# Kernel tuning notes

Measured on AMD Instinct MI355X. Metric: run time of the kernel, lower is better.

Reference implementation:

```python
import jax, jax.numpy as jnp
import numpy as np

T, H_IN = 2048, 84
HID = 256
NA = 18


def _conv(x, w, b, stride):
    # x: [N,C,H,W], w: [O,I,kh,kw]
    y = jax.lax.conv_general_dilated(
        x, w, window_strides=(stride, stride), padding='VALID',
        dimension_numbers=('NCHW', 'OIHW', 'NCHW'))
    return jax.nn.relu(y + b[None, :, None, None])


def setup_inputs() -> dict:
    key = jax.random.key(0)
    ks = jax.random.split(key, 17)
    p = lambda k, shape, s=0.05: (jax.random.normal(k, shape, jnp.float32) * s)
    return {
        'input_frames': jax.random.uniform(ks[0], (T, 1, H_IN, H_IN), jnp.float32),
        'conv1_w': p(ks[1], (32, 1, 8, 8)),   'conv1_b': p(ks[2], (32,)),
        'conv2_w': p(ks[3], (64, 32, 4, 4)),  'conv2_b': p(ks[4], (64,)),
        'conv3_w': p(ks[5], (256, 64, 3, 3)), 'conv3_b': p(ks[6], (256,)),
        'attn_w1': p(ks[7], (HID, HID)),      'attn_b1': p(ks[8], (HID,)),
        'attn_w2': p(ks[9], (HID, HID)),      'attn_b2': p(ks[10], (HID,)),
        'lstm_w_ih': p(ks[11], (4 * HID, HID)), 'lstm_w_hh': p(ks[12], (4 * HID, HID)),
        'lstm_b_ih': p(ks[13], (4 * HID,)),     'lstm_b_hh': p(ks[14], (4 * HID,)),
        'q_w': p(ks[15], (NA, HID)),          'q_b': p(ks[16], (NA,)),
    }


def reference(input_frames, conv1_w, conv1_b, conv2_w, conv2_b, conv3_w, conv3_b,
              attn_w1, attn_b1, attn_w2, attn_b2,
              lstm_w_ih, lstm_w_hh, lstm_b_ih, lstm_b_hh, q_w, q_b):
    # CNN over all frames at once (loop in torch was over frames; math identical)
    x = _conv(input_frames, conv1_w, conv1_b, 4)   # [T,32,20,20]
    x = _conv(x, conv2_w, conv2_b, 2)              # [T,64,9,9]
    fm = _conv(x, conv3_w, conv3_b, 1)             # [T,256,7,7]
    t, c, hh, ww = fm.shape
    # build_vector: vectors[i, ch] = fm[ch, y, x], i = y*W + x
    vecs = fm.reshape(t, c, hh * ww).transpose(0, 2, 1)  # [T,49,256]

    def step(carry, v):
        h, cc = carry  # [256], [256]
        # additive attention; softmax over the 256 feature dim per spatial vector
        s = jnp.tanh(v @ attn_w1.T + attn_b1 + h)              # [49,256]
        w = jax.nn.softmax(s @ attn_w2.T + attn_b2, axis=-1)   # [49,256]
        ctx = jnp.sum(w * v, axis=0)                           # [256]
        # single-layer LSTM cell, torch gate order i,f,g,o
        gates = ctx @ lstm_w_ih.T + lstm_b_ih + h @ lstm_w_hh.T + lstm_b_hh
        i, f, g, o = jnp.split(gates, 4)
        c_new = jax.nn.sigmoid(f) * cc + jax.nn.sigmoid(i) * jnp.tanh(g)
        h_new = jax.nn.sigmoid(o) * jnp.tanh(c_new)
        return (h_new, c_new), None

    h0 = jnp.zeros((HID,), fm.dtype)
    (h_T, _), _ = jax.lax.scan(step, (h0, h0), vecs)
    q = h_T @ q_w.T + q_b          # [18]
    return q[None, :]              # [1, nr_actions], matches torch output
```

## Files before the change

### kernel.cpp

```cpp
#include <hip/hip_runtime.h>
#include <hip/hip_bf16.h>
#include <math.h>


#define T_FRAMES 2048
#define NI 49
#define HID 256
#define NA 18
#define NWG 8

typedef __bf16 v8bf __attribute__((ext_vector_type(8)));
typedef float v4f __attribute__((ext_vector_type(4)));

static constexpr size_t OFF_FM1   = 0;
static constexpr size_t OFF_FM2   = 104857600;
static constexpr size_t OFF_VECS  = 147324928;
static constexpr size_t OFF_W2B   = 250085376;
static constexpr size_t OFF_WIHB  = OFF_W2B  + 131072;
static constexpr size_t OFF_WHHB  = OFF_WIHB + 524288;
static constexpr size_t OFF_W1T   = OFF_WHHB + 524288;
static constexpr size_t OFF_HBUF  = OFF_FM2;
static constexpr size_t OFF_CPUB  = OFF_FM2 + 2048;

__global__ void prep_weights(const float* __restrict__ w2, const float* __restrict__ wih,
                             const float* __restrict__ whh, const float* __restrict__ w1,
                             __bf16* w2b, __bf16* wihb, __bf16* whhb, float* w1t) {
  int idx = blockIdx.x * 256 + threadIdx.x;
  int stride = gridDim.x * 256;
  for (int i = idx; i < 65536; i += stride) w2b[i] = (__bf16)w2[i];
  for (int i = idx; i < 262144; i += stride) wihb[i] = (__bf16)wih[i];
  for (int i = idx; i < 262144; i += stride) whhb[i] = (__bf16)whh[i];
  for (int i = idx; i < 65536; i += stride) {
    int r = i >> 8, c = i & 255;
    w1t[c * 256 + r] = w1[i];
  }
}

__global__ void conv1_k(const float* __restrict__ x, const float* __restrict__ w,
                        const float* __restrict__ b, float* __restrict__ y) {
  int idx = blockIdx.x * 256 + threadIdx.x;
  if (idx >= T_FRAMES * 32 * 20 * 20) return;
  int xx = idx % 20, yy = (idx / 20) % 20, o = (idx / 400) % 32, t = idx / 12800;
  const float* xp = x + t * 7056 + yy * 4 * 84 + xx * 4;
  const float* wp = w + o * 64;
  float acc = b[o];
  #pragma unroll
  for (int ky = 0; ky < 8; ky++)
    #pragma unroll
    for (int kx = 0; kx < 8; kx++)
      acc += xp[ky * 84 + kx] * wp[ky * 8 + kx];
  y[idx] = fmaxf(acc, 0.f);
}

__global__ __launch_bounds__(256) void conv2_k(const float* __restrict__ fm1, const float* __restrict__ w,
                                               const float* __restrict__ b, float* __restrict__ fm2) {
  __shared__ float xs[32 * 400];
  int t = blockIdx.x, tid = threadIdx.x;
  for (int i = tid; i < 12800; i += 256) xs[i] = fm1[t * 12800 + i];
  __syncthreads();
  int o = tid >> 2, q = tid & 3;
  int p0 = q * 21, p1 = (p0 + 21 < 81) ? p0 + 21 : 81;
  int ob[21];
  #pragma unroll
  for (int i2 = 0; i2 < 21; i2++) {
    int p = p0 + i2; if (p > 80) p = 80;
    int yy = p / 9, xx2 = p - yy * 9;
    ob[i2] = yy * 40 + xx2 * 2;
  }
  float acc[21];
  #pragma unroll
  for (int i2 = 0; i2 < 21; i2++) acc[i2] = 0.f;
  for (int c = 0; c < 32; c++) {
    int cbase = c * 400;
    for (int ky = 0; ky < 4; ky++)
      for (int kx = 0; kx < 4; kx++) {
        float wgt = w[((o * 32 + c) * 4 + ky) * 4 + kx];
        int kyo = ky * 20 + kx;
        #pragma unroll
        for (int i2 = 0; i2 < 21; i2++)
          acc[i2] += wgt * xs[cbase + ob[i2] + kyo];
      }
  }
  float bo = b[o];
  #pragma unroll
  for (int i2 = 0; i2 < 21; i2++) {
    int p = p0 + i2;
    if (p < p1) fm2[t * 5184 + o * 81 + p] = fmaxf(acc[i2] + bo, 0.f);
  }
}

__global__ __launch_bounds__(256) void conv3_k(const float* __restrict__ fm2, const float* __restrict__ w,
                                               const float* __restrict__ b, float* __restrict__ vecs) {
  __shared__ float xs[64 * 81];
  __shared__ float ws4[256][37];
  int t = blockIdx.x, tid = threadIdx.x;
  for (int i = tid; i < 64 * 81; i += 256) xs[i] = fm2[t * 5184 + i];
  float acc[49];
  #pragma unroll
  for (int i = 0; i < 49; i++) acc[i] = 0.f;
  for (int c0 = 0; c0 < 64; c0 += 4) {
    __syncthreads();
    for (int i = tid; i < 256 * 36; i += 256) {
      int oo = i / 36, j = i - oo * 36;
      ws4[oo][j] = w[oo * 576 + c0 * 9 + j];
    }
    __syncthreads();
    for (int cc = 0; cc < 4; cc++)
      for (int ky = 0; ky < 3; ky++)
        for (int kx = 0; kx < 3; kx++) {
          float wgt = ws4[tid][cc * 9 + ky * 3 + kx];
          const float* xp = &xs[(c0 + cc) * 81 + ky * 9 + kx];
          #pragma unroll
          for (int yy = 0; yy < 7; yy++)
            #pragma unroll
            for (int xx = 0; xx < 7; xx++)
              acc[yy * 7 + xx] += wgt * xp[yy * 9 + xx];
        }
  }
  float bo = b[tid];
  for (int i = 0; i < 49; i++)
    vecs[(t * 49 + i) * 256 + tid] = fmaxf(acc[i] + bo, 0.f);
}

__global__ __launch_bounds__(256) void aprep_k(const float* __restrict__ vecs, const float* __restrict__ w1t,
                                               const float* __restrict__ b1, float* __restrict__ A) {
  __shared__ float vs[49][256];
  int t = blockIdx.x, tid = threadIdx.x;
  for (int i = tid; i < 49 * 256; i += 256) vs[i >> 8][i & 255] = vecs[t * 12544 + i];
  __syncthreads();
  float acc[49];
  #pragma unroll
  for (int i = 0; i < 49; i++) acc[i] = 0.f;
  for (int k = 0; k < 256; k++) {
    float wgt = w1t[k * 256 + tid];
    #pragma unroll
    for (int i = 0; i < 49; i++) acc[i] += vs[i][k] * wgt;
  }
  float bb = b1[tid];
  for (int i = 0; i < 49; i++) A[(t * 49 + i) * 256 + tid] = acc[i] + bb;
}

__global__ void init_comm(unsigned long long* hbuf, unsigned long long* cpub) {
  int idx = blockIdx.x * 256 + threadIdx.x;
  if (idx < 256) hbuf[idx] = 0ull;
  if (idx < NWG * 128) cpub[idx] = 0ull;
}

__device__ __forceinline__ float tanh_fast(float x) {
  float e = __expf(2.f * x);
  return 1.f - 2.f * __builtin_amdgcn_rcpf(e + 1.f);
}
__device__ __forceinline__ float sigm_fast(float x) {
  return __builtin_amdgcn_rcpf(1.f + __expf(-x));
}

__global__ __launch_bounds__(256, 1) void scan_k(
    const float* __restrict__ A, const float* __restrict__ vecs,
    const __bf16* __restrict__ w2b, const __bf16* __restrict__ wihb, const __bf16* __restrict__ whhb,
    const float* __restrict__ b2g, const float* __restrict__ bihg, const float* __restrict__ bhhg,
    const float* __restrict__ qw, const float* __restrict__ qb,
    unsigned long long* hbuf, unsigned long long* cpub, float* out) {
  const int w = blockIdx.x;

  __shared__ __bf16 Ss[16][264];
  __shared__ float hs[HID];
  __shared__ __bf16 hbf[HID];
  __shared__ float Wt[8][HID];
  __shared__ float cxp[8][HID];
  __shared__ float b2s[HID];
  __shared__ float gb[4][32];
  __shared__ unsigned cpl[128];

  const int tid = threadIdx.x;
  const int lane = tid & 63;
  const int wv = tid >> 6;
  const int quad = lane >> 4;
  const int l15 = lane & 15;
  const int r0 = 6 * w;
  const int nr = (w < 7) ? 6 : 7;
  const int prow = tid >> 5;
  const int pcol = (tid & 31) * 8;

  for (int i = tid; i < 16 * 264; i += 256) (&Ss[0][0])[i] = (__bf16)0.f;
  for (int i = tid; i < 8 * HID; i += 256) (&cxp[0][0])[i] = 0.f;
  b2s[tid] = b2g[tid];
  hs[tid] = 0.f;
  hbf[tid] = (__bf16)0.f;
  float cbias[4];
  if (tid < 32) {
    #pragma unroll
    for (int g = 0; g < 4; g++) {
      int row = 256 * g + 32 * w + tid;
      cbias[g] = bihg[row] + bhhg[row];
    }
  }
  float creg = 0.f;

  v8bf BW2[4][8];
  #pragma unroll
  for (int ntl = 0; ntl < 4; ntl++) {
    const int row = wv * 64 + ntl * 16 + l15;
    #pragma unroll
    for (int k = 0; k < 8; k++)
      BW2[ntl][k] = *(const v8bf*)(w2b + row * 256 + k * 32 + quad * 8);
  }
  v8bf BIH[2][8], BHH[2][8];
  #pragma unroll
  for (int nt = 0; nt < 2; nt++) {
    const int row = 256 * wv + 32 * w + nt * 16 + l15;
    #pragma unroll
    for (int k = 0; k < 8; k++) {
      BIH[nt][k] = *(const v8bf*)(wihb + row * 256 + k * 32 + quad * 8);
      BHH[nt][k] = *(const v8bf*)(whhb + row * 256 + k * 32 + quad * 8);
    }
  }
  __syncthreads();

  for (int t = 0; t < T_FRAMES; t++) {
    int rr = r0 + prow; if (rr > 48) rr = 48;
    const float* Ap = A + ((long)t * NI + rr) * HID + pcol;
    const float* Vp = vecs + ((long)t * NI + rr) * HID + pcol;
    const float4 a40 = *(const float4*)(Ap);
    const float4 a41 = *(const float4*)(Ap + 4);
    const float4 v40 = *(const float4*)(Vp);
    const float4 v41 = *(const float4*)(Vp + 4);

    if (t > 0) {
      const unsigned tgt = (unsigned)t;
      unsigned long long pk =
          __hip_atomic_load(&hbuf[tid], __ATOMIC_RELAXED, __HIP_MEMORY_SCOPE_AGENT);
      int guard = 0;
      while ((unsigned)(pk >> 32) < tgt && ++guard < 5000000) {
        __builtin_amdgcn_s_sleep(1);
        pk = __hip_atomic_load(&hbuf[tid], __ATOMIC_RELAXED, __HIP_MEMORY_SCOPE_AGENT);
      }
      float hv = __uint_as_float((unsigned)pk);
      hs[tid] = hv;
      hbf[tid] = (__bf16)hv;
      __syncthreads();
    }

    if (prow < nr) {
      const float* hp = &hs[pcol];
      v8bf sv;
      sv[0] = (__bf16)tanh_fast(a40.x + hp[0]);
      sv[1] = (__bf16)tanh_fast(a40.y + hp[1]);
      sv[2] = (__bf16)tanh_fast(a40.z + hp[2]);
      sv[3] = (__bf16)tanh_fast(a40.w + hp[3]);
      sv[4] = (__bf16)tanh_fast(a41.x + hp[4]);
      sv[5] = (__bf16)tanh_fast(a41.y + hp[5]);
      sv[6] = (__bf16)tanh_fast(a41.z + hp[6]);
      sv[7] = (__bf16)tanh_fast(a41.w + hp[7]);
      *(v8bf*)&Ss[prow][pcol] = sv;
    }
    __syncthreads();

    v4f acc[4];
    #pragma unroll
    for (int ntl = 0; ntl < 4; ntl++) acc[ntl] = (v4f){0.f, 0.f, 0.f, 0.f};
    #pragma unroll
    for (int k = 0; k < 8; k++) {
      const v8bf av = *(const v8bf*)&Ss[l15][k * 32 + quad * 8];
      #pragma unroll
      for (int ntl = 0; ntl < 4; ntl++)
        acc[ntl] = __builtin_amdgcn_mfma_f32_16x16x32_bf16(av, BW2[ntl][k], acc[ntl], 0, 0, 0);
    }
    if (quad < 2) {
      #pragma unroll
      for (int ntl = 0; ntl < 4; ntl++) {
        const int col = wv * 64 + ntl * 16 + l15;
        const float bb = b2s[col];
        #pragma unroll
        for (int reg = 0; reg < 4; reg++)
          Wt[quad * 4 + reg][col] = acc[ntl][reg] + bb;
      }
    }
    __syncthreads();

    if (prow < nr) {
      float x[8];
      *(float4*)&x[0] = *(const float4*)&Wt[prow][pcol];
      *(float4*)&x[4] = *(const float4*)&Wt[prow][pcol + 4];
      float m = x[0];
      #pragma unroll
      for (int i = 1; i < 8; i++) m = fmaxf(m, x[i]);
      #pragma unroll
      for (int off = 16; off; off >>= 1) m = fmaxf(m, __shfl_xor(m, off, 64));
      float e[8], sm = 0.f;
      #pragma unroll
      for (int i = 0; i < 8; i++) { e[i] = __expf(x[i] - m); sm += e[i]; }
      #pragma unroll
      for (int off = 16; off; off >>= 1) sm += __shfl_xor(sm, off, 64);
      const float inv = __builtin_amdgcn_rcpf(sm);
      cxp[prow][pcol + 0] = e[0] * inv * v40.x;
      cxp[prow][pcol + 1] = e[1] * inv * v40.y;
      cxp[prow][pcol + 2] = e[2] * inv * v40.z;
      cxp[prow][pcol + 3] = e[3] * inv * v40.w;
      cxp[prow][pcol + 4] = e[4] * inv * v41.x;
      cxp[prow][pcol + 5] = e[5] * inv * v41.y;
      cxp[prow][pcol + 6] = e[6] * inv * v41.z;
      cxp[prow][pcol + 7] = e[7] * inv * v41.w;
    }
    __syncthreads();

    float cp = 0.f;
    #pragma unroll
    for (int r = 0; r < 8; r++) cp += cxp[r][tid];
    float cpo = __shfl_xor(cp, 1, 64);
    if ((tid & 1) == 0) {
      union { __bf16 b; unsigned short s; } lo, hi;
      lo.b = (__bf16)cp; hi.b = (__bf16)cpo;
      unsigned word = ((unsigned)hi.s << 16) | (unsigned)lo.s;
      unsigned long long pk =
          ((unsigned long long)(unsigned)(t + 1) << 32) | (unsigned long long)word;
      __hip_atomic_store(&cpub[w * 128 + (tid >> 1)], pk, __ATOMIC_RELAXED, __HIP_MEMORY_SCOPE_AGENT);
      cpl[tid >> 1] = word;
    }
    __syncthreads();

    v4f gacc[2];
    gacc[0] = (v4f){0.f, 0.f, 0.f, 0.f};
    gacc[1] = (v4f){0.f, 0.f, 0.f, 0.f};
    #pragma unroll
    for (int k = 0; k < 8; k++) {
      v8bf hf;
      #pragma unroll
      for (int z = 0; z < 8; z++) hf[z] = (__bf16)0.f;
      if (l15 == 0) hf = *(const v8bf*)&hbf[k * 32 + quad * 8];
      gacc[0] = __builtin_amdgcn_mfma_f32_16x16x32_bf16(hf, BHH[0][k], gacc[0], 0, 0, 0);
      gacc[1] = __builtin_amdgcn_mfma_f32_16x16x32_bf16(hf, BHH[1][k], gacc[1], 0, 0, 0);
    }

    unsigned long long g[8][4];
    const unsigned ctgt = (unsigned)(t + 1);
    const bool remote = (l15 < NWG) && (l15 != w);
    {
      int guard = 0;
      while (true) {
        bool ok = true;
        if (remote) {
          const unsigned long long* src = cpub + l15 * 128 + quad * 4;
          #pragma unroll
          for (int k = 0; k < 8; k++)
            #pragma unroll
            for (int q2 = 0; q2 < 4; q2++) {
              g[k][q2] = __hip_atomic_load(&src[k * 16 + q2], __ATOMIC_RELAXED, __HIP_MEMORY_SCOPE_AGENT);
              ok &= ((unsigned)(g[k][q2] >> 32) >= ctgt);
            }
        }
        if (__all(ok) || ++guard > 5000000) break;
        __builtin_amdgcn_s_sleep(1);
      }
    }

    #pragma unroll
    for (int k = 0; k < 8; k++) {
      union { unsigned u[4]; v8bf v; } pf;
      if (remote) {
        pf.u[0] = (unsigned)g[k][0]; pf.u[1] = (unsigned)g[k][1];
        pf.u[2] = (unsigned)g[k][2]; pf.u[3] = (unsigned)g[k][3];
      } else if (l15 == w) {
        pf.u[0] = cpl[k * 16 + quad * 4 + 0];
        pf.u[1] = cpl[k * 16 + quad * 4 + 1];
        pf.u[2] = cpl[k * 16 + quad * 4 + 2];
        pf.u[3] = cpl[k * 16 + quad * 4 + 3];
      } else {
        pf.u[0] = pf.u[1] = pf.u[2] = pf.u[3] = 0u;
      }
      gacc[0] = __builtin_amdgcn_mfma_f32_16x16x32_bf16(pf.v, BIH[0][k], gacc[0], 0, 0, 0);
      gacc[1] = __builtin_amdgcn_mfma_f32_16x16x32_bf16(pf.v, BIH[1][k], gacc[1], 0, 0, 0);
    }
    #pragma unroll
    for (int nt = 0; nt < 2; nt++) {
      float tot = gacc[nt][0] + gacc[nt][1] + gacc[nt][2] + gacc[nt][3];
      tot += __shfl_xor(tot, 16, 64);
      tot += __shfl_xor(tot, 32, 64);
      if (lane < 16) gb[wv][nt * 16 + lane] = tot;
    }
    __syncthreads();

    if (tid < 32) {
      float gi = gb[0][tid] + cbias[0];
      float gf = gb[1][tid] + cbias[1];
      float gg = gb[2][tid] + cbias[2];
      float go = gb[3][tid] + cbias[3];
      float si = sigm_fast(gi);
      float sf = sigm_fast(gf);
      float so = sigm_fast(go);
      creg = sf * creg + si * tanh_fast(gg);
      float hn = so * tanh_fast(creg);
      unsigned long long pk = ((unsigned long long)(unsigned)(t + 1) << 32) |
                              (unsigned long long)__float_as_uint(hn);
      __hip_atomic_store(&hbuf[32 * w + tid], pk, __ATOMIC_RELAXED, __HIP_MEMORY_SCOPE_AGENT);
    }
  }

  if (w == 0) {
    const unsigned tgt = (unsigned)T_FRAMES;
    unsigned long long pk =
        __hip_atomic_load(&hbuf[tid], __ATOMIC_RELAXED, __HIP_MEMORY_SCOPE_AGENT);
    int guard = 0;
    while ((unsigned)(pk >> 32) < tgt && ++guard < 5000000) {
      __builtin_amdgcn_s_sleep(1);
      pk = __hip_atomic_load(&hbuf[tid], __ATOMIC_RELAXED, __HIP_MEMORY_SCOPE_AGENT);
    }
    hs[tid] = __uint_as_float((unsigned)pk);
    __syncthreads();
    if (tid < NA) {
      float acc = qb[tid];
      for (int k = 0; k < HID; k++) acc += hs[k] * qw[tid * HID + k];
      out[tid] = acc;
    }
  }
}

extern "C" void kernel_launch(void* const* d_in, const int* in_sizes, int n_in,
                              void* d_out, int out_size, void* d_ws, size_t ws_size,
                              hipStream_t stream) {
  const float* frames = (const float*)d_in[0];
  const float* c1w = (const float*)d_in[1];
  const float* c1b = (const float*)d_in[2];
  const float* c2w = (const float*)d_in[3];
  const float* c2b = (const float*)d_in[4];
  const float* c3w = (const float*)d_in[5];
  const float* c3b = (const float*)d_in[6];
  const float* aw1 = (const float*)d_in[7];
  const float* ab1 = (const float*)d_in[8];
  const float* aw2 = (const float*)d_in[9];
  const float* ab2 = (const float*)d_in[10];
  const float* wih = (const float*)d_in[11];
  const float* whh = (const float*)d_in[12];
  const float* bih = (const float*)d_in[13];
  const float* bhh = (const float*)d_in[14];
  const float* qw  = (const float*)d_in[15];
  const float* qb  = (const float*)d_in[16];

  char* ws = (char*)d_ws;
  float*  fm1   = (float*)(ws + OFF_FM1);
  float*  A     = (float*)(ws + OFF_FM1);
  float*  fm2   = (float*)(ws + OFF_FM2);
  float*  vecs  = (float*)(ws + OFF_VECS);
  __bf16* w2b   = (__bf16*)(ws + OFF_W2B);
  __bf16* wihb  = (__bf16*)(ws + OFF_WIHB);
  __bf16* whhb  = (__bf16*)(ws + OFF_WHHB);
  float*  w1t   = (float*)(ws + OFF_W1T);
  unsigned long long* hbuf = (unsigned long long*)(ws + OFF_HBUF);
  unsigned long long* cpub = (unsigned long long*)(ws + OFF_CPUB);

  prep_weights<<<256, 256, 0, stream>>>(aw2, wih, whh, aw1, w2b, wihb, whhb, w1t);
  conv1_k<<<102400, 256, 0, stream>>>(frames, c1w, c1b, fm1);
  conv2_k<<<T_FRAMES, 256, 0, stream>>>(fm1, c2w, c2b, fm2);
  conv3_k<<<T_FRAMES, 256, 0, stream>>>(fm2, c3w, c3b, vecs);
  aprep_k<<<T_FRAMES, 256, 0, stream>>>(vecs, w1t, ab1, A);
  init_comm<<<4, 256, 0, stream>>>(hbuf, cpub);
  scan_k<<<NWG, 256, 0, stream>>>(A, vecs, w2b, wihb, whhb, ab2, bih, bhh, qw, qb,
                                  hbuf, cpub, (float*)d_out);
}
```

Baseline: 15.29 ms.

## Compute full attention context redundantly per workgroup, dropping cross-workgroup context exchange

Each of the 8 workgroups now computes attention over all 49 spatial rows (four 16-row MFMA tiles) instead of a 6-7 row slice. The per-step exchange of partial context sums through global memory, with its second spin-wait barrier, is removed. Only the hidden-state exchange is left as a cross-workgroup sync per step. The cost is about 8x redundant attention work per workgroup, more global loads per step, and much larger LDS use.

```diff
diff --git a/kernel.cpp b/kernel.cpp
--- a/kernel.cpp
+++ b/kernel.cpp
@@ -19,8 +19,7 @@
 static constexpr size_t OFF_WIHB  = OFF_W2B  + 131072;
 static constexpr size_t OFF_WHHB  = OFF_WIHB + 524288;
 static constexpr size_t OFF_W1T   = OFF_WHHB + 524288;
-static constexpr size_t OFF_HBUF  = OFF_FM2;
-static constexpr size_t OFF_CPUB  = OFF_FM2 + 2048;
+static constexpr size_t OFF_COMM  = OFF_FM2;
 
 __global__ void prep_weights(const float* __restrict__ w2, const float* __restrict__ wih,
                              const float* __restrict__ whh, const float* __restrict__ w1,
@@ -140,10 +139,10 @@
   for (int i = 0; i < 49; i++) A[(t * 49 + i) * 256 + tid] = acc[i] + bb;
 }
 
-__global__ void init_comm(unsigned long long* hbuf, unsigned long long* cpub) {
+__global__ void init_comm(unsigned long long* comm) {
   int idx = blockIdx.x * 256 + threadIdx.x;
-  if (idx < 256) hbuf[idx] = 0ull;
-  if (idx < NWG * 128) cpub[idx] = 0ull;
+  if (idx < 256)
+    __hip_atomic_store(&comm[idx], 0ull, __ATOMIC_RELAXED, __HIP_MEMORY_SCOPE_AGENT);
 }
 
 __device__ __forceinline__ float tanh_fast(float x) {
@@ -159,30 +158,27 @@
     const __bf16* __restrict__ w2b, const __bf16* __restrict__ wihb, const __bf16* __restrict__ whhb,
     const float* __restrict__ b2g, const float* __restrict__ bihg, const float* __restrict__ bhhg,
     const float* __restrict__ qw, const float* __restrict__ qb,
-    unsigned long long* hbuf, unsigned long long* cpub, float* out) {
+    unsigned long long* hbuf, float* out) {
   const int w = blockIdx.x;
 
-  __shared__ __bf16 Ss[16][264];
+  __shared__ __bf16 Ss[64][264];
+  __shared__ float Wt[64][260];
+  __shared__ float cxp[8][HID];
   __shared__ float hs[HID];
   __shared__ __bf16 hbf[HID];
-  __shared__ float Wt[8][HID];
-  __shared__ float cxp[8][HID];
+  __shared__ __bf16 ctxbf[HID];
   __shared__ float b2s[HID];
   __shared__ float gb[4][32];
-  __shared__ unsigned cpl[128];
 
   const int tid = threadIdx.x;
   const int lane = tid & 63;
   const int wv = tid >> 6;
   const int quad = lane >> 4;
   const int l15 = lane & 15;
-  const int r0 = 6 * w;
-  const int nr = (w < 7) ? 6 : 7;
   const int prow = tid >> 5;
   const int pcol = (tid & 31) * 8;
 
-  for (int i = tid; i < 16 * 264; i += 256) (&Ss[0][0])[i] = (__bf16)0.f;
-  for (int i = tid; i < 8 * HID; i += 256) (&cxp[0][0])[i] = 0.f;
+  for (int i = tid; i < 64 * 264; i += 256) (&Ss[0][0])[i] = (__bf16)0.f;
   b2s[tid] = b2g[tid];
   hs[tid] = 0.f;
   hbf[tid] = (__bf16)0.f;
@@ -217,20 +213,26 @@
   __syncthreads();
 
   for (int t = 0; t < T_FRAMES; t++) {
-    int rr = r0 + prow; if (rr > 48) rr = 48;
-    const float* Ap = A + ((long)t * NI + rr) * HID + pcol;
-    const float* Vp = vecs + ((long)t * NI + rr) * HID + pcol;
-    const float4 a40 = *(const float4*)(Ap);
-    const float4 a41 = *(const float4*)(Ap + 4);
-    const float4 v40 = *(const float4*)(Vp);
-    const float4 v41 = *(const float4*)(Vp + 4);
+    const long base = (long)t * NI * HID;
+    float4 aa0[8], aa1[8], vv0[8], vv1[8];
+    #pragma unroll
+    for (int i = 0; i < 8; i++) {
+      int row = prow + 8 * i;
+      int ra = (row < NI) ? row : (NI - 1);
+      const float* Ap = A + base + (long)ra * HID + pcol;
+      const float* Vp = vecs + base + (long)ra * HID + pcol;
+      aa0[i] = *(const float4*)(Ap);
+      aa1[i] = *(const float4*)(Ap + 4);
+      vv0[i] = *(const float4*)(Vp);
+      vv1[i] = *(const float4*)(Vp + 4);
+    }
 
     if (t > 0) {
       const unsigned tgt = (unsigned)t;
       unsigned long long pk =
           __hip_atomic_load(&hbuf[tid], __ATOMIC_RELAXED, __HIP_MEMORY_SCOPE_AGENT);
-      int guard = 0;
-      while ((unsigned)(pk >> 32) < tgt && ++guard < 5000000) {
+      int gd = 0;
+      while ((unsigned)(pk >> 32) != tgt && ++gd < 5000000) {
         __builtin_amdgcn_s_sleep(1);
         pk = __hip_atomic_load(&hbuf[tid], __ATOMIC_RELAXED, __HIP_MEMORY_SCOPE_AGENT);
       }
@@ -240,81 +242,94 @@
       __syncthreads();
     }
 
-    if (prow < nr) {
+    {
       const float* hp = &hs[pcol];
-      v8bf sv;
-      sv[0] = (__bf16)tanh_fast(a40.x + hp[0]);
-      sv[1] = (__bf16)tanh_fast(a40.y + hp[1]);
-      sv[2] = (__bf16)tanh_fast(a40.z + hp[2]);
-      sv[3] = (__bf16)tanh_fast(a40.w + hp[3]);
-      sv[4] = (__bf16)tanh_fast(a41.x + hp[4]);
-      sv[5] = (__bf16)tanh_fast(a41.y + hp[5]);
-      sv[6] = (__bf16)tanh_fast(a41.z + hp[6]);
-      sv[7] = (__bf16)tanh_fast(a41.w + hp[7]);
-      *(v8bf*)&Ss[prow][pcol] = sv;
-    }
-    __syncthreads();
-
-    v4f acc[4];
-    #pragma unroll
-    for (int ntl = 0; ntl < 4; ntl++) acc[ntl] = (v4f){0.f, 0.f, 0.f, 0.f};
-    #pragma unroll
-    for (int k = 0; k < 8; k++) {
-      const v8bf av = *(const v8bf*)&Ss[l15][k * 32 + quad * 8];
-      #pragma unroll
-      for (int ntl = 0; ntl < 4; ntl++)
-        acc[ntl] = __builtin_amdgcn_mfma_f32_16x16x32_bf16(av, BW2[ntl][k], acc[ntl], 0, 0, 0);
-    }
-    if (quad < 2) {
+      float h0 = hp[0], h1 = hp[1], h2 = hp[2], h3 = hp[3];
+      float h4 = hp[4], h5 = hp[5], h6 = hp[6], h7 = hp[7];
+      #pragma unroll
+      for (int i = 0; i < 8; i++) {
+        int row = prow + 8 * i;
+        if (row < NI) {
+          v8bf sv;
+          sv[0] = (__bf16)tanh_fast(aa0[i].x + h0);
+          sv[1] = (__bf16)tanh_fast(aa0[i].y + h1);
+          sv[2] = (__bf16)tanh_fast(aa0[i].z + h2);
+          sv[3] = (__bf16)tanh_fast(aa0[i].w + h3);
+          sv[4] = (__bf16)tanh_fast(aa1[i].x + h4);
+          sv[5] = (__bf16)tanh_fast(aa1[i].y + h5);
+          sv[6] = (__bf16)tanh_fast(aa1[i].z + h6);
+          sv[7] = (__bf16)tanh_fast(aa1[i].w + h7);
+          *(v8bf*)&Ss[row][pcol] = sv;
+        }
+      }
+    }
+    __syncthreads();
+
+    #pragma unroll
+    for (int rt = 0; rt < 4; rt++) {
+      v4f acc[4];
+      #pragma unroll
+      for (int ntl = 0; ntl < 4; ntl++) acc[ntl] = (v4f){0.f, 0.f, 0.f, 0.f};
+      #pragma unroll
+      for (int k = 0; k < 8; k++) {
+        const v8bf av = *(const v8bf*)&Ss[rt * 16 + l15][k * 32 + quad * 8];
+        #pragma unroll
+        for (int ntl = 0; ntl < 4; ntl++)
+          acc[ntl] = __builtin_amdgcn_mfma_f32_16x16x32_bf16(av, BW2[ntl][k], acc[ntl], 0, 0, 0);
+      }
       #pragma unroll
       for (int ntl = 0; ntl < 4; ntl++) {
         const int col = wv * 64 + ntl * 16 + l15;
         const float bb = b2s[col];
         #pragma unroll
         for (int reg = 0; reg < 4; reg++)
-          Wt[quad * 4 + reg][col] = acc[ntl][reg] + bb;
-      }
-    }
-    __syncthreads();
-
-    if (prow < nr) {
-      float x[8];
-      *(float4*)&x[0] = *(const float4*)&Wt[prow][pcol];
-      *(float4*)&x[4] = *(const float4*)&Wt[prow][pcol + 4];
-      float m = x[0];
-      #pragma unroll
-      for (int i = 1; i < 8; i++) m = fmaxf(m, x[i]);
-      #pragma unroll
-      for (int off = 16; off; off >>= 1) m = fmaxf(m, __shfl_xor(m, off, 64));
-      float e[8], sm = 0.f;
-      #pragma unroll
-      for (int i = 0; i < 8; i++) { e[i] = __expf(x[i] - m); sm += e[i]; }
-      #pragma unroll
-      for (int off = 16; off; off >>= 1) sm += __shfl_xor(sm, off, 64);
-      const float inv = __builtin_amdgcn_rcpf(sm);
-      cxp[prow][pcol + 0] = e[0] * inv * v40.x;
-      cxp[prow][pcol + 1] = e[1] * inv * v40.y;
-      cxp[prow][pcol + 2] = e[2] * inv * v40.z;
-      cxp[prow][pcol + 3] = e[3] * inv * v40.w;
-      cxp[prow][pcol + 4] = e[4] * inv * v41.x;
-      cxp[prow][pcol + 5] = e[5] * inv * v41.y;
-      cxp[prow][pcol + 6] = e[6] * inv * v41.z;
-      cxp[prow][pcol + 7] = e[7] * inv * v41.w;
-    }
-    __syncthreads();
-
-    float cp = 0.f;
-    #pragma unroll
-    for (int r = 0; r < 8; r++) cp += cxp[r][tid];
-    float cpo = __shfl_xor(cp, 1, 64);
-    if ((tid & 1) == 0) {
-      union { __bf16 b; unsigned short s; } lo, hi;
-      lo.b = (__bf16)cp; hi.b = (__bf16)cpo;
-      unsigned word = ((unsigned)hi.s << 16) | (unsigned)lo.s;
-      unsigned long long pk =
-          ((unsigned long long)(unsigned)(t + 1) << 32) | (unsigned long long)word;
-      __hip_atomic_store(&cpub[w * 128 + (tid >> 1)], pk, __ATOMIC_RELAXED, __HIP_MEMORY_SCOPE_AGENT);
-      cpl[tid >> 1] = word;
+          Wt[rt * 16 + quad * 4 + reg][col] = acc[ntl][reg] + bb;
+      }
+    }
+    __syncthreads();
+
+    {
+      float cacc[8];
+      #pragma unroll
+      for (int j = 0; j < 8; j++) cacc[j] = 0.f;
+      #pragma unroll
+      for (int i = 0; i < 8; i++) {
+        int row = prow + 8 * i;
+        if (row < NI) {
+          float x[8];
+          *(float4*)&x[0] = *(const float4*)&Wt[row][pcol];
+          *(float4*)&x[4] = *(const float4*)&Wt[row][pcol + 4];
+          float m = x[0];
+          #pragma unroll
+          for (int j = 1; j < 8; j++) m = fmaxf(m, x[j]);
+          #pragma unroll
+          for (int off = 16; off; off >>= 1) m = fmaxf(m, __shfl_xor(m, off, 64));
+          float e[8], sm = 0.f;
+          #pragma unroll
+          for (int j = 0; j < 8; j++) { e[j] = __expf(x[j] - m); sm += e[j]; }
+          #pragma unroll
+          for (int off = 16; off; off >>= 1) sm += __shfl_xor(sm, off, 64);
+          const float inv = __builtin_amdgcn_rcpf(sm);
+          cacc[0] += e[0] * inv * vv0[i].x;
+          cacc[1] += e[1] * inv * vv0[i].y;
+          cacc[2] += e[2] * inv * vv0[i].z;
+          cacc[3] += e[3] * inv * vv0[i].w;
+          cacc[4] += e[4] * inv * vv1[i].x;
+          cacc[5] += e[5] * inv * vv1[i].y;
+          cacc[6] += e[6] * inv * vv1[i].z;
+          cacc[7] += e[7] * inv * vv1[i].w;
+        }
+      }
+      #pragma unroll
+      for (int j = 0; j < 8; j++) cxp[prow][pcol + j] = cacc[j];
+    }
+    __syncthreads();
+
+    {
+      float cp = 0.f;
+      #pragma unroll
+      for (int r = 0; r < 8; r++) cp += cxp[r][tid];
+      ctxbf[tid] = (__bf16)cp;
     }
     __syncthreads();
 
@@ -323,52 +338,17 @@
     gacc[1] = (v4f){0.f, 0.f, 0.f, 0.f};
     #pragma unroll
     for (int k = 0; k < 8; k++) {
-      v8bf hf;
-      #pragma unroll
-      for (int z = 0; z < 8; z++) hf[z] = (__bf16)0.f;
-      if (l15 == 0) hf = *(const v8bf*)&hbf[k * 32 + quad * 8];
+      v8bf hf, cf;
+      #pragma unroll
+      for (int z = 0; z < 8; z++) { hf[z] = (__bf16)0.f; cf[z] = (__bf16)0.f; }
+      if (l15 == 0) {
+        hf = *(const v8bf*)&hbf[k * 32 + quad * 8];
+        cf = *(const v8bf*)&ctxbf[k * 32 + quad * 8];
+      }
       gacc[0] = __builtin_amdgcn_mfma_f32_16x16x32_bf16(hf, BHH[0][k], gacc[0], 0, 0, 0);
       gacc[1] = __builtin_amdgcn_mfma_f32_16x16x32_bf16(hf, BHH[1][k], gacc[1], 0, 0, 0);
-    }
-
-    unsigned long long g[8][4];
-    const unsigned ctgt = (unsigned)(t + 1);
-    const bool remote = (l15 < NWG) && (l15 != w);
-    {
-      int guard = 0;
-      while (true) {
-        bool ok = true;
-        if (remote) {
-          const unsigned long long* src = cpub + l15 * 128 + quad * 4;
-          #pragma unroll
-          for (int k = 0; k < 8; k++)
-            #pragma unroll
-            for (int q2 = 0; q2 < 4; q2++) {
-              g[k][q2] = __hip_atomic_load(&src[k * 16 + q2], __ATOMIC_RELAXED, __HIP_MEMORY_SCOPE_AGENT);
-              ok &= ((unsigned)(g[k][q2] >> 32) >= ctgt);
-            }
-        }
-        if (__all(ok) || ++guard > 5000000) break;
-        __builtin_amdgcn_s_sleep(1);
-      }
-    }
-
-    #pragma unroll
-    for (int k = 0; k < 8; k++) {
-      union { unsigned u[4]; v8bf v; } pf;
-      if (remote) {
-        pf.u[0] = (unsigned)g[k][0]; pf.u[1] = (unsigned)g[k][1];
-        pf.u[2] = (unsigned)g[k][2]; pf.u[3] = (unsigned)g[k][3];
-      } else if (l15 == w) {
-        pf.u[0] = cpl[k * 16 + quad * 4 + 0];
-        pf.u[1] = cpl[k * 16 + quad * 4 + 1];
-        pf.u[2] = cpl[k * 16 + quad * 4 + 2];
-        pf.u[3] = cpl[k * 16 + quad * 4 + 3];
-      } else {
-        pf.u[0] = pf.u[1] = pf.u[2] = pf.u[3] = 0u;
-      }
-      gacc[0] = __builtin_amdgcn_mfma_f32_16x16x32_bf16(pf.v, BIH[0][k], gacc[0], 0, 0, 0);
-      gacc[1] = __builtin_amdgcn_mfma_f32_16x16x32_bf16(pf.v, BIH[1][k], gacc[1], 0, 0, 0);
+      gacc[0] = __builtin_amdgcn_mfma_f32_16x16x32_bf16(cf, BIH[0][k], gacc[0], 0, 0, 0);
+      gacc[1] = __builtin_amdgcn_mfma_f32_16x16x32_bf16(cf, BIH[1][k], gacc[1], 0, 0, 0);
     }
     #pragma unroll
     for (int nt = 0; nt < 2; nt++) {
@@ -399,8 +379,8 @@
     const unsigned tgt = (unsigned)T_FRAMES;
     unsigned long long pk =
         __hip_atomic_load(&hbuf[tid], __ATOMIC_RELAXED, __HIP_MEMORY_SCOPE_AGENT);
-    int guard = 0;
-    while ((unsigned)(pk >> 32) < tgt && ++guard < 5000000) {
+    int gd = 0;
+    while ((unsigned)(pk >> 32) != tgt && ++gd < 5000000) {
       __builtin_amdgcn_s_sleep(1);
       pk = __hip_atomic_load(&hbuf[tid], __ATOMIC_RELAXED, __HIP_MEMORY_SCOPE_AGENT);
     }
@@ -444,15 +424,14 @@
   __bf16* wihb  = (__bf16*)(ws + OFF_WIHB);
   __bf16* whhb  = (__bf16*)(ws + OFF_WHHB);
   float*  w1t   = (float*)(ws + OFF_W1T);
-  unsigned long long* hbuf = (unsigned long long*)(ws + OFF_HBUF);
-  unsigned long long* cpub = (unsigned long long*)(ws + OFF_CPUB);
+  unsigned long long* hbuf = (unsigned long long*)(ws + OFF_COMM);
 
   prep_weights<<<256, 256, 0, stream>>>(aw2, wih, whh, aw1, w2b, wihb, whhb, w1t);
   conv1_k<<<102400, 256, 0, stream>>>(frames, c1w, c1b, fm1);
   conv2_k<<<T_FRAMES, 256, 0, stream>>>(fm1, c2w, c2b, fm2);
   conv3_k<<<T_FRAMES, 256, 0, stream>>>(fm2, c3w, c3b, vecs);
   aprep_k<<<T_FRAMES, 256, 0, stream>>>(vecs, w1t, ab1, A);
-  init_comm<<<4, 256, 0, stream>>>(hbuf, cpub);
+  init_comm<<<1, 256, 0, stream>>>(hbuf);
   scan_k<<<NWG, 256, 0, stream>>>(A, vecs, w2b, wihb, whhb, ab2, bih, bhh, qw, qb,
-                                  hbuf, cpub, (float*)d_out);
-}
+                                  hbuf, (float*)d_out);
+}
```

Measured after the change: 21.06 ms. 1.38x slower.

## Fuse CNN stages into per-frame producer blocks overlapping the recurrent scan

Applied to the files above, without the earlier changes.

Merges conv1, conv2, conv3 and the attention pre-projection into a single persistent mega-kernel. Blocks 0-7 run the sequential LSTM/attention scan, and the remaining 2048 blocks each compute one frame's CNN features in shared memory and publish a per-frame ready flag. The scan blocks poll those flags in batches of 64 frames, so feature extraction overlaps the latency-bound recurrence and the fm1/fm2 round trips through global memory go away. The risks are that the scan blocks must be resident before the producers saturate the GPU, and that the large shared-memory footprint (about 117KB plus scan buffers) limits how many producer blocks fit on each CU.

```diff
diff --git a/kernel.cpp b/kernel.cpp
--- a/kernel.cpp
+++ b/kernel.cpp
@@ -19,8 +19,8 @@
 static constexpr size_t OFF_WIHB  = OFF_W2B  + 131072;
 static constexpr size_t OFF_WHHB  = OFF_WIHB + 524288;
 static constexpr size_t OFF_W1T   = OFF_WHHB + 524288;
-static constexpr size_t OFF_HBUF  = OFF_FM2;
-static constexpr size_t OFF_CPUB  = OFF_FM2 + 2048;
+static constexpr size_t OFF_COMM  = OFF_FM2;
+static constexpr int COMM_WORDS = 256 + NWG * 128 + T_FRAMES;
 
 __global__ void prep_weights(const float* __restrict__ w2, const float* __restrict__ wih,
                              const float* __restrict__ whh, const float* __restrict__ w1,
@@ -36,114 +36,10 @@
   }
 }
 
-__global__ void conv1_k(const float* __restrict__ x, const float* __restrict__ w,
-                        const float* __restrict__ b, float* __restrict__ y) {
+__global__ void init_comm(unsigned long long* comm) {
   int idx = blockIdx.x * 256 + threadIdx.x;
-  if (idx >= T_FRAMES * 32 * 20 * 20) return;
-  int xx = idx % 20, yy = (idx / 20) % 20, o = (idx / 400) % 32, t = idx / 12800;
-  const float* xp = x + t * 7056 + yy * 4 * 84 + xx * 4;
-  const float* wp = w + o * 64;
-  float acc = b[o];
-  #pragma unroll
-  for (int ky = 0; ky < 8; ky++)
-    #pragma unroll
-    for (int kx = 0; kx < 8; kx++)
-      acc += xp[ky * 84 + kx] * wp[ky * 8 + kx];
-  y[idx] = fmaxf(acc, 0.f);
-}
-
-__global__ __launch_bounds__(256) void conv2_k(const float* __restrict__ fm1, const float* __restrict__ w,
-                                               const float* __restrict__ b, float* __restrict__ fm2) {
-  __shared__ float xs[32 * 400];
-  int t = blockIdx.x, tid = threadIdx.x;
-  for (int i = tid; i < 12800; i += 256) xs[i] = fm1[t * 12800 + i];
-  __syncthreads();
-  int o = tid >> 2, q = tid & 3;
-  int p0 = q * 21, p1 = (p0 + 21 < 81) ? p0 + 21 : 81;
-  int ob[21];
-  #pragma unroll
-  for (int i2 = 0; i2 < 21; i2++) {
-    int p = p0 + i2; if (p > 80) p = 80;
-    int yy = p / 9, xx2 = p - yy * 9;
-    ob[i2] = yy * 40 + xx2 * 2;
-  }
-  float acc[21];
-  #pragma unroll
-  for (int i2 = 0; i2 < 21; i2++) acc[i2] = 0.f;
-  for (int c = 0; c < 32; c++) {
-    int cbase = c * 400;
-    for (int ky = 0; ky < 4; ky++)
-      for (int kx = 0; kx < 4; kx++) {
-        float wgt = w[((o * 32 + c) * 4 + ky) * 4 + kx];
-        int kyo = ky * 20 + kx;
-        #pragma unroll
-        for (int i2 = 0; i2 < 21; i2++)
-          acc[i2] += wgt * xs[cbase + ob[i2] + kyo];
-      }
-  }
-  float bo = b[o];
-  #pragma unroll
-  for (int i2 = 0; i2 < 21; i2++) {
-    int p = p0 + i2;
-    if (p < p1) fm2[t * 5184 + o * 81 + p] = fmaxf(acc[i2] + bo, 0.f);
-  }
-}
-
-__global__ __launch_bounds__(256) void conv3_k(const float* __restrict__ fm2, const float* __restrict__ w,
-                                               const float* __restrict__ b, float* __restrict__ vecs) {
-  __shared__ float xs[64 * 81];
-  __shared__ float ws4[256][37];
-  int t = blockIdx.x, tid = threadIdx.x;
-  for (int i = tid; i < 64 * 81; i += 256) xs[i] = fm2[t * 5184 + i];
-  float acc[49];
-  #pragma unroll
-  for (int i = 0; i < 49; i++) acc[i] = 0.f;
-  for (int c0 = 0; c0 < 64; c0 += 4) {
-    __syncthreads();
-    for (int i = tid; i < 256 * 36; i += 256) {
-      int oo = i / 36, j = i - oo * 36;
-      ws4[oo][j] = w[oo * 576 + c0 * 9 + j];
-    }
-    __syncthreads();
-    for (int cc = 0; cc < 4; cc++)
-      for (int ky = 0; ky < 3; ky++)
-        for (int kx = 0; kx < 3; kx++) {
-          float wgt = ws4[tid][cc * 9 + ky * 3 + kx];
-          const float* xp = &xs[(c0 + cc) * 81 + ky * 9 + kx];
-          #pragma unroll
-          for (int yy = 0; yy < 7; yy++)
-            #pragma unroll
-            for (int xx = 0; xx < 7; xx++)
-              acc[yy * 7 + xx] += wgt * xp[yy * 9 + xx];
-        }
-  }
-  float bo = b[tid];
-  for (int i = 0; i < 49; i++)
-    vecs[(t * 49 + i) * 256 + tid] = fmaxf(acc[i] + bo, 0.f);
-}
-
-__global__ __launch_bounds__(256) void aprep_k(const float* __restrict__ vecs, const float* __restrict__ w1t,
-                                               const float* __restrict__ b1, float* __restrict__ A) {
-  __shared__ float vs[49][256];
-  int t = blockIdx.x, tid = threadIdx.x;
-  for (int i = tid; i < 49 * 256; i += 256) vs[i >> 8][i & 255] = vecs[t * 12544 + i];
-  __syncthreads();
-  float acc[49];
-  #pragma unroll
-  for (int i = 0; i < 49; i++) acc[i] = 0.f;
-  for (int k = 0; k < 256; k++) {
-    float wgt = w1t[k * 256 + tid];
-    #pragma unroll
-    for (int i = 0; i < 49; i++) acc[i] += vs[i][k] * wgt;
-  }
-  float bb = b1[tid];
-  for (int i = 0; i < 49; i++) A[(t * 49 + i) * 256 + tid] = acc[i] + bb;
-}
-
-__global__ void init_comm(unsigned long long* hbuf, unsigned long long* cpub) {
-  int idx = blockIdx.x * 256 + threadIdx.x;
-  if (idx < 256) hbuf[idx] = 0ull;
-  if (idx < NWG * 128) cpub[idx] = 0ull;
+  if (idx < COMM_WORDS)
+    __hip_atomic_store(&comm[idx], 0ull, __ATOMIC_RELAXED, __HIP_MEMORY_SCOPE_AGENT);
 }
 
 __device__ __forceinline__ float tanh_fast(float x) {
@@ -154,14 +50,20 @@
   return __builtin_amdgcn_rcpf(1.f + __expf(-x));
 }
 
-__global__ __launch_bounds__(256, 1) void scan_k(
-    const float* __restrict__ A, const float* __restrict__ vecs,
-    const __bf16* __restrict__ w2b, const __bf16* __restrict__ wihb, const __bf16* __restrict__ whhb,
-    const float* __restrict__ b2g, const float* __restrict__ bihg, const float* __restrict__ bhhg,
+__global__ __launch_bounds__(256, 1) void mega_k(
+    const float* frames,
+    const float* __restrict__ c1w, const float* __restrict__ c1b,
+    const float* __restrict__ c2w, const float* __restrict__ c2b,
+    const float* __restrict__ c3w, const float* __restrict__ c3b,
+    const float* __restrict__ w1t, const float* __restrict__ ab1,
+    float* A, float* vecs,
+    const __bf16* __restrict__ w2b, const __bf16* __restrict__ wihb,
+    const __bf16* __restrict__ whhb,
+    const float* __restrict__ b2g, const float* __restrict__ bihg,
+    const float* __restrict__ bhhg,
     const float* __restrict__ qw, const float* __restrict__ qb,
-    unsigned long long* hbuf, unsigned long long* cpub, float* out) {
-  const int w = blockIdx.x;
-
+    unsigned long long* hbuf, unsigned long long* cpub, unsigned long long* flags,
+    float* out) {
   __shared__ __bf16 Ss[16][264];
   __shared__ float hs[HID];
   __shared__ __bf16 hbf[HID];
@@ -170,8 +72,119 @@
   __shared__ float b2s[HID];
   __shared__ float gb[4][32];
   __shared__ unsigned cpl[128];
+  __shared__ __attribute__((aligned(16))) float pbuf_f[29376];
 
   const int tid = threadIdx.x;
+
+  if (blockIdx.x >= 8) {
+    const int f = (int)blockIdx.x - 8;
+    float* xin    = pbuf_f;
+    float* fm1s   = pbuf_f + 7104;
+    float* ws4p   = pbuf_f + 19904;
+    float* fm2s   = xin;
+    float* vecs_s = fm1s;
+
+    for (int i = tid; i < 7056; i += 256) xin[i] = frames[(long)f * 7056 + i];
+    __syncthreads();
+    for (int i = tid; i < 12800; i += 256) {
+      int xx = i % 20, yy = (i / 20) % 20, o = i / 400;
+      const float* xp = xin + yy * 4 * 84 + xx * 4;
+      const float* wp = c1w + o * 64;
+      float acc = c1b[o];
+      #pragma unroll
+      for (int ky = 0; ky < 8; ky++)
+        #pragma unroll
+        for (int kx = 0; kx < 8; kx++)
+          acc += xp[ky * 84 + kx] * wp[ky * 8 + kx];
+      fm1s[i] = fmaxf(acc, 0.f);
+    }
+    __syncthreads();
+
+    {
+      int o = tid >> 2, q = tid & 3;
+      int p0 = q * 21, p1 = (p0 + 21 < 81) ? p0 + 21 : 81;
+      int ob[21];
+      #pragma unroll
+      for (int i2 = 0; i2 < 21; i2++) {
+        int p = p0 + i2; if (p > 80) p = 80;
+        int yy = p / 9, xx2 = p - yy * 9;
+        ob[i2] = yy * 40 + xx2 * 2;
+      }
+      float acc[21];
+      #pragma unroll
+      for (int i2 = 0; i2 < 21; i2++) acc[i2] = 0.f;
+      for (int c = 0; c < 32; c++) {
+        int cbase = c * 400;
+        for (int ky = 0; ky < 4; ky++)
+          for (int kx = 0; kx < 4; kx++) {
+            float wgt = c2w[((o * 32 + c) * 4 + ky) * 4 + kx];
+            int kyo = ky * 20 + kx;
+            #pragma unroll
+            for (int i2 = 0; i2 < 21; i2++)
+              acc[i2] += wgt * fm1s[cbase + ob[i2] + kyo];
+          }
+      }
+      float bo = c2b[o];
+      #pragma unroll
+      for (int i2 = 0; i2 < 21; i2++) {
+        int p = p0 + i2;
+        if (p < p1) fm2s[o * 81 + p] = fmaxf(acc[i2] + bo, 0.f);
+      }
+    }
+
+    {
+      float acc[49];
+      #pragma unroll
+      for (int i = 0; i < 49; i++) acc[i] = 0.f;
+      for (int c0 = 0; c0 < 64; c0 += 4) {
+        __syncthreads();
+        for (int i = tid; i < 256 * 36; i += 256) {
+          int oo = i / 36, j = i - oo * 36;
+          ws4p[oo * 37 + j] = c3w[oo * 576 + c0 * 9 + j];
+        }
+        __syncthreads();
+        for (int cc = 0; cc < 4; cc++)
+          for (int ky = 0; ky < 3; ky++)
+            for (int kx = 0; kx < 3; kx++) {
+              float wgt = ws4p[tid * 37 + cc * 9 + ky * 3 + kx];
+              const float* xp = &fm2s[(c0 + cc) * 81 + ky * 9 + kx];
+              #pragma unroll
+              for (int yy = 0; yy < 7; yy++)
+                #pragma unroll
+                for (int xx = 0; xx < 7; xx++)
+                  acc[yy * 7 + xx] += wgt * xp[yy * 9 + xx];
+            }
+      }
+      float bo = c3b[tid];
+      for (int i = 0; i < 49; i++) {
+        float v = fmaxf(acc[i] + bo, 0.f);
+        vecs[((long)f * 49 + i) * 256 + tid] = v;
+        vecs_s[i * 256 + tid] = v;
+      }
+    }
+    __syncthreads();
+
+    {
+      float acc2[49];
+      #pragma unroll
+      for (int i = 0; i < 49; i++) acc2[i] = 0.f;
+      for (int k = 0; k < 256; k++) {
+        float wgt = w1t[k * 256 + tid];
+        #pragma unroll
+        for (int i = 0; i < 49; i++) acc2[i] += vecs_s[i * 256 + k] * wgt;
+      }
+      float bb = ab1[tid];
+      for (int i = 0; i < 49; i++)
+        A[((long)f * 49 + i) * 256 + tid] = acc2[i] + bb;
+    }
+    __syncthreads();
+    if (tid == 0)
+      __hip_atomic_store(&flags[f], (unsigned long long)(f + 1),
+                         __ATOMIC_RELEASE, __HIP_MEMORY_SCOPE_AGENT);
+    return;
+  }
+
+  const int w = (int)blockIdx.x;
   const int lane = tid & 63;
   const int wv = tid >> 6;
   const int quad = lane >> 4;
@@ -216,7 +229,23 @@
   }
   __syncthreads();
 
+  int ready = 0;
+
   for (int t = 0; t < T_FRAMES; t++) {
+    if (t >= ready) {
+      int idx = t + lane; if (idx > T_FRAMES - 1) idx = T_FRAMES - 1;
+      const unsigned long long want = (unsigned long long)(idx + 1);
+      unsigned long long fv =
+          __hip_atomic_load(&flags[idx], __ATOMIC_RELAXED, __HIP_MEMORY_SCOPE_AGENT);
+      int gd = 0;
+      while (!__all(fv == want) && ++gd < 5000000) {
+        __builtin_amdgcn_s_sleep(8);
+        fv = __hip_atomic_load(&flags[idx], __ATOMIC_RELAXED, __HIP_MEMORY_SCOPE_AGENT);
+      }
+      (void)__hip_atomic_load(&flags[idx], __ATOMIC_ACQUIRE, __HIP_MEMORY_SCOPE_AGENT);
+      ready = t + 64;
+    }
+
     int rr = r0 + prow; if (rr > 48) rr = 48;
     const float* Ap = A + ((long)t * NI + rr) * HID + pcol;
     const float* Vp = vecs + ((long)t * NI + rr) * HID + pcol;
@@ -229,8 +258,8 @@
       const unsigned tgt = (unsigned)t;
       unsigned long long pk =
           __hip_atomic_load(&hbuf[tid], __ATOMIC_RELAXED, __HIP_MEMORY_SCOPE_AGENT);
-      int guard = 0;
-      while ((unsigned)(pk >> 32) < tgt && ++guard < 5000000) {
+      int gd = 0;
+      while ((unsigned)(pk >> 32) < tgt && ++gd < 5000000) {
         __builtin_amdgcn_s_sleep(1);
         pk = __hip_atomic_load(&hbuf[tid], __ATOMIC_RELAXED, __HIP_MEMORY_SCOPE_AGENT);
       }
@@ -335,7 +364,7 @@
     const unsigned ctgt = (unsigned)(t + 1);
     const bool remote = (l15 < NWG) && (l15 != w);
     {
-      int guard = 0;
+      int gd = 0;
       while (true) {
         bool ok = true;
         if (remote) {
@@ -348,7 +377,7 @@
               ok &= ((unsigned)(g[k][q2] >> 32) >= ctgt);
             }
         }
-        if (__all(ok) || ++guard > 5000000) break;
+        if (__all(ok) || ++gd > 5000000) break;
         __builtin_amdgcn_s_sleep(1);
       }
     }
@@ -399,8 +428,8 @@
     const unsigned tgt = (unsigned)T_FRAMES;
     unsigned long long pk =
         __hip_atomic_load(&hbuf[tid], __ATOMIC_RELAXED, __HIP_MEMORY_SCOPE_AGENT);
-    int guard = 0;
-    while ((unsigned)(pk >> 32) < tgt && ++guard < 5000000) {
+    int gd = 0;
+    while ((unsigned)(pk >> 32) < tgt && ++gd < 5000000) {
       __builtin_amdgcn_s_sleep(1);
       pk = __hip_atomic_load(&hbuf[tid], __ATOMIC_RELAXED, __HIP_MEMORY_SCOPE_AGENT);
     }
@@ -436,23 +465,21 @@
   const float* qb  = (const float*)d_in[16];
 
   char* ws = (char*)d_ws;
-  float*  fm1   = (float*)(ws + OFF_FM1);
   float*  A     = (float*)(ws + OFF_FM1);
-  float*  fm2   = (float*)(ws + OFF_FM2);
   float*  vecs  = (float*)(ws + OFF_VECS);
   __bf16* w2b   = (__bf16*)(ws + OFF_W2B);
   __bf16* wihb  = (__bf16*)(ws + OFF_WIHB);
   __bf16* whhb  = (__bf16*)(ws + OFF_WHHB);
   float*  w1t   = (float*)(ws + OFF_W1T);
-  unsigned long long* hbuf = (unsigned long long*)(ws + OFF_HBUF);
-  unsigned long long* cpub = (unsigned long long*)(ws + OFF_CPUB);
+  unsigned long long* comm = (unsigned long long*)(ws + OFF_COMM);
+  unsigned long long* hbuf  = comm;
+  unsigned long long* cpub  = comm + 256;
+  unsigned long long* flags = comm + 1280;
 
   prep_weights<<<256, 256, 0, stream>>>(aw2, wih, whh, aw1, w2b, wihb, whhb, w1t);
-  conv1_k<<<102400, 256, 0, stream>>>(frames, c1w, c1b, fm1);
-  conv2_k<<<T_FRAMES, 256, 0, stream>>>(fm1, c2w, c2b, fm2);
-  conv3_k<<<T_FRAMES, 256, 0, stream>>>(fm2, c3w, c3b, vecs);
-  aprep_k<<<T_FRAMES, 256, 0, stream>>>(vecs, w1t, ab1, A);
-  init_comm<<<4, 256, 0, stream>>>(hbuf, cpub);
-  scan_k<<<NWG, 256, 0, stream>>>(A, vecs, w2b, wihb, whhb, ab2, bih, bhh, qw, qb,
-                                  hbuf, cpub, (float*)d_out);
-}
+  init_comm<<<13, 256, 0, stream>>>(comm);
+  mega_k<<<8 + T_FRAMES, 256, 0, stream>>>(
+      frames, c1w, c1b, c2w, c2b, c3w, c3b, w1t, ab1,
+      A, vecs, w2b, wihb, whhb, ab2, bih, bhh, qw, qb,
+      hbuf, cpub, flags, (float*)d_out);
+}
```

New measurement: 14.13 ms. 1.08x faster.
